# Optimization experiments

Hardware: AMD Instinct MI355X
Metric: run time of the kernel (lower is better)

## Reference

```python
import jax, jax.numpy as jnp
import numpy as np

D_MODEL = 1024
NHEAD = 16
HEAD_DIM = D_MODEL // NHEAD
D_FF = 4 * D_MODEL
B, L = 2, 2048
EPS = 1e-5


def layer_norm(x, g, b):
    mu = jnp.mean(x, axis=-1, keepdims=True)
    var = jnp.mean(jnp.square(x - mu), axis=-1, keepdims=True)
    return (x - mu) * jax.lax.rsqrt(var + EPS) * g + b


def setup_inputs() -> dict:
    key = jax.random.key(0)
    ks = jax.random.split(key, 12)
    s = 1.0 / np.sqrt(D_MODEL)
    inp = {
        "x": jax.random.normal(ks[0], (B, L, D_MODEL), jnp.float32),
        "mask": jnp.tril(jnp.ones((L, L), jnp.int32)),  # causal mask; 0 => masked
        "Wq": jax.random.normal(ks[1], (D_MODEL, D_MODEL), jnp.float32) * s,
        "bq": jnp.zeros((D_MODEL,), jnp.float32),
        "Wk": jax.random.normal(ks[2], (D_MODEL, D_MODEL), jnp.float32) * s,
        "bk": jnp.zeros((D_MODEL,), jnp.float32),
        "Wv": jax.random.normal(ks[3], (D_MODEL, D_MODEL), jnp.float32) * s,
        "bv": jnp.zeros((D_MODEL,), jnp.float32),
        "Wo": jax.random.normal(ks[4], (D_MODEL, D_MODEL), jnp.float32) * s,
        "bo": jnp.zeros((D_MODEL,), jnp.float32),
        "g1": jnp.ones((D_MODEL,), jnp.float32),
        "b1": jnp.zeros((D_MODEL,), jnp.float32),
        "g2": jnp.ones((D_MODEL,), jnp.float32),
        "b2": jnp.zeros((D_MODEL,), jnp.float32),
        "W1": jax.random.normal(ks[5], (D_MODEL, D_FF), jnp.float32) * s,
        "bf1": jnp.zeros((D_FF,), jnp.float32),
        "W2": jax.random.normal(ks[6], (D_FF, D_MODEL), jnp.float32) * (1.0 / np.sqrt(D_FF)),
        "bf2": jnp.zeros((D_MODEL,), jnp.float32),
    }
    return inp


def reference(x, mask, Wq, bq, Wk, bk, Wv, bv, Wo, bo, g1, b1, g2, b2, W1, bf1, W2, bf2):
    # Pre-norm attention (dropout = identity in eval mode)
    nx = layer_norm(x, g1, b1)
    Bb, Ll, Dd = nx.shape
    def heads(t):
        return t.reshape(Bb, Ll, NHEAD, HEAD_DIM).transpose(0, 2, 1, 3)  # [B,H,L,hd]
    q = heads(nx @ Wq + bq)
    k = heads(nx @ Wk + bk)
    v = heads(nx @ Wv + bv)
    scale = 1.0 / np.sqrt(HEAD_DIM)
    attn = jnp.einsum("bhqd,bhkd->bhqk", q, k) * scale  # [B,H,L,L]
    attn = jnp.where(mask[:Ll, :Ll] == 0, jnp.float32(-1e9), attn)
    attn = jax.nn.softmax(attn, axis=-1)
    attn_out = jnp.einsum("bhqk,bhkd->bhqd", attn, v)
    attn_out = attn_out.transpose(0, 2, 1, 3).reshape(Bb, Ll, Dd)
    x = x + (attn_out @ Wo + bo)
    # Pre-norm FFN with exact GELU (torch nn.GELU default)
    nx2 = layer_norm(x, g2, b2)
    h = jax.nn.gelu(nx2 @ W1 + bf1, approximate=False)
    x = x + (h @ W2 + bf2)
    return x
```

## Files before the change

### kernel.cpp

```cpp
#include <hip/hip_runtime.h>
#include <hip/hip_bf16.h>

__device__ __forceinline__ float bfbits2f(unsigned short u) {
  return __uint_as_float(((unsigned int)u) << 16);
}
__device__ __forceinline__ unsigned short f2bfbits(float f) {
  unsigned int x = __float_as_uint(f);
  unsigned int r = (x + 0x7FFFu + ((x >> 16) & 1u)) >> 16;
  return (unsigned short)r;
}

typedef short bf16x8 __attribute__((ext_vector_type(8)));
typedef float f32x4 __attribute__((ext_vector_type(4)));

__device__ __forceinline__ void gload_lds16(const unsigned short* g, unsigned short* l) {
  __builtin_amdgcn_global_load_lds((const __attribute__((address_space(1))) unsigned int*)g,
                                   (__attribute__((address_space(3))) unsigned int*)l, 16, 0, 0);
}

__global__ __launch_bounds__(256) void transpose_cast_k(const float* __restrict__ in,
                                                        unsigned short* __restrict__ out,
                                                        int K, int N) {
  __shared__ float tile[32][33];
  int n0 = blockIdx.x * 32, k0 = blockIdx.y * 32;
  int tx = threadIdx.x, ty = threadIdx.y;
#pragma unroll
  for (int j = 0; j < 32; j += 8)
    tile[ty + j][tx] = in[(size_t)(k0 + ty + j) * N + n0 + tx];
  __syncthreads();
#pragma unroll
  for (int j = 0; j < 32; j += 8)
    out[(size_t)(n0 + ty + j) * K + k0 + tx] = f2bfbits(tile[tx][ty + j]);
}

__global__ __launch_bounds__(256) void transpose_cast4_k(const float* __restrict__ w0,
                                                         const float* __restrict__ w1,
                                                         const float* __restrict__ w2,
                                                         const float* __restrict__ w3,
                                                         unsigned short* __restrict__ o012,
                                                         unsigned short* __restrict__ o3) {
  __shared__ float tile[32][33];
  int z = blockIdx.z;
  const float* in = (z == 0) ? w0 : (z == 1) ? w1 : (z == 2) ? w2 : w3;
  unsigned short* out = (z < 3) ? (o012 + (size_t)z * 1024 * 1024) : o3;
  int n0 = blockIdx.x * 32, k0 = blockIdx.y * 32;
  int tx = threadIdx.x, ty = threadIdx.y;
#pragma unroll
  for (int j = 0; j < 32; j += 8)
    tile[ty + j][tx] = in[(size_t)(k0 + ty + j) * 1024 + n0 + tx];
  __syncthreads();
#pragma unroll
  for (int j = 0; j < 32; j += 8)
    out[(size_t)(n0 + ty + j) * 1024 + k0 + tx] = f2bfbits(tile[tx][ty + j]);
}

__global__ void concat_bias_k(const float* __restrict__ bq, const float* __restrict__ bk,
                              const float* __restrict__ bv, float* __restrict__ out) {
  int i = blockIdx.x * 256 + threadIdx.x;
  if (i < 1024) {
    out[i] = bq[i];
    out[1024 + i] = bk[i];
    out[2048 + i] = bv[i];
  }
}

__global__ __launch_bounds__(256) void ln_k(const float* __restrict__ x,
                                            const float* __restrict__ g,
                                            const float* __restrict__ bb,
                                            unsigned short* __restrict__ out) {
  __shared__ float red[8];
  int row = blockIdx.x, tid = threadIdx.x;
  int lane = tid & 63, wv = tid >> 6;
  float4 v = reinterpret_cast<const float4*>(x + (size_t)row * 1024)[tid];
  float s = v.x + v.y + v.z + v.w;
#pragma unroll
  for (int off = 32; off >= 1; off >>= 1) s += __shfl_xor(s, off, 64);
  if (lane == 0) red[wv] = s;
  __syncthreads();
  float mu = (red[0] + red[1] + red[2] + red[3]) * (1.0f / 1024.0f);
  float a0 = v.x - mu, a1 = v.y - mu, a2 = v.z - mu, a3 = v.w - mu;
  float sq = a0 * a0 + a1 * a1 + a2 * a2 + a3 * a3;
#pragma unroll
  for (int off = 32; off >= 1; off >>= 1) sq += __shfl_xor(sq, off, 64);
  if (lane == 0) red[4 + wv] = sq;
  __syncthreads();
  float var = (red[4] + red[5] + red[6] + red[7]) * (1.0f / 1024.0f);
  float rstd = rsqrtf(var + 1e-5f);
  float4 gv = reinterpret_cast<const float4*>(g)[tid];
  float4 bv = reinterpret_cast<const float4*>(bb)[tid];
  ushort4 u;
  u.x = f2bfbits(a0 * rstd * gv.x + bv.x);
  u.y = f2bfbits(a1 * rstd * gv.y + bv.y);
  u.z = f2bfbits(a2 * rstd * gv.z + bv.z);
  u.w = f2bfbits(a3 * rstd * gv.w + bv.w);
  *reinterpret_cast<ushort4*>(out + (size_t)row * 1024 + tid * 4) = u;
}

template <int MODE>
__global__ __launch_bounds__(256) void gemm_bt_k(const unsigned short* __restrict__ A,
                                                 const unsigned short* __restrict__ BT,
                                                 const float* __restrict__ bias,
                                                 const float* __restrict__ resid,
                                                 void* __restrict__ Cout,
                                                 int M, int N, int K) {
  __shared__ unsigned short As[128 * 64];
  __shared__ unsigned short Bs[128 * 64];
  int tid = threadIdx.x;
  int wid = tid >> 6, lane = tid & 63;
  int m0 = blockIdx.x * 128, n0 = blockIdx.y * 128;
  int wr = wid >> 1, wc = wid & 1;
  int cl = lane & 15, g = lane >> 4;

  f32x4 acc[4][4];
#pragma unroll
  for (int i = 0; i < 4; i++)
#pragma unroll
    for (int j = 0; j < 4; j++) acc[i][j] = {0.f, 0.f, 0.f, 0.f};

  for (int k0 = 0; k0 < K; k0 += 64) {
#pragma unroll
    for (int i = 0; i < 4; ++i) {
      int c = i * 256 + tid;
      int r = c >> 3;
      int cc = (c & 7) * 8;
      gload_lds16(&A[(size_t)(m0 + r) * K + k0 + cc], &As[(i * 256 + wid * 64) * 8]);
      gload_lds16(&BT[(size_t)(n0 + r) * K + k0 + cc], &Bs[(i * 256 + wid * 64) * 8]);
    }
    __syncthreads();
#pragma unroll
    for (int kk = 0; kk < 64; kk += 32) {
      bf16x8 af[4], bfr[4];
#pragma unroll
      for (int mt = 0; mt < 4; mt++)
        af[mt] = *reinterpret_cast<const bf16x8*>(&As[(wr * 64 + mt * 16 + cl) * 64 + kk + g * 8]);
#pragma unroll
      for (int nt = 0; nt < 4; nt++)
        bfr[nt] = *reinterpret_cast<const bf16x8*>(&Bs[(wc * 64 + nt * 16 + cl) * 64 + kk + g * 8]);
#pragma unroll
      for (int mt = 0; mt < 4; mt++)
#pragma unroll
        for (int nt = 0; nt < 4; nt++)
          acc[mt][nt] = __builtin_amdgcn_mfma_f32_16x16x32_bf16(af[mt], bfr[nt], acc[mt][nt], 0, 0, 0);
    }
    __syncthreads();
  }

#pragma unroll
  for (int mt = 0; mt < 4; mt++) {
#pragma unroll
    for (int nt = 0; nt < 4; nt++) {
#pragma unroll
      for (int r = 0; r < 4; r++) {
        int gr = m0 + wr * 64 + mt * 16 + g * 4 + r;
        int gc = n0 + wc * 64 + nt * 16 + cl;
        float v = acc[mt][nt][r] + bias[gc];
        if constexpr (MODE == 1) {
          v += resid[(size_t)gr * N + gc];
          ((float*)Cout)[(size_t)gr * N + gc] = v;
        } else if constexpr (MODE == 2) {
          v = 0.5f * v * (1.0f + erff(v * 0.70710678118654752f));
          ((unsigned short*)Cout)[(size_t)gr * N + gc] = f2bfbits(v);
        } else {
          ((unsigned short*)Cout)[(size_t)gr * N + gc] = f2bfbits(v);
        }
      }
    }
  }
}

__global__ __launch_bounds__(512) void attn_k(const unsigned short* __restrict__ qkv,
                                              unsigned short* __restrict__ out) {
  __shared__ unsigned short Ks[2][64 * 64];
  __shared__ unsigned short Vt[64 * 64];
  __shared__ unsigned short Ps[8][16 * 64];

  const int L = 2048, RS = 3072;
  const float SCALE = 0.125f * 1.44269504f;
  int tid = threadIdx.x;
  int wid = tid >> 6, lane = tid & 63;
  int qt = (int)gridDim.x - 1 - (int)blockIdx.x;
  int h = blockIdx.y, b = blockIdx.z;
  int q0 = qt * 128;
  int qw = q0 + wid * 16;
  int g = lane >> 4;
  int cl = lane & 15;

  const unsigned short* kbase = qkv + (size_t)(b * L) * RS + 1024 + h * 64;
  const unsigned short* vbase = kbase + 1024;

  const unsigned short* qbase = qkv + (size_t)(b * L + qw + cl) * RS + h * 64 + g * 8;
  bf16x8 qf0 = *reinterpret_cast<const bf16x8*>(qbase);
  bf16x8 qf1 = *reinterpret_cast<const bf16x8*>(qbase + 32);

  int kr = tid >> 3, kch = tid & 7;
  size_t ksrc_off = (size_t)kr * RS + ((kch ^ (kr & 7)) * 8);
  int vk = tid & 63, vd0 = (tid >> 6) * 8;
  int vaddr[8];
#pragma unroll
  for (int j = 0; j < 8; ++j) {
    int d = vd0 + j;
    vaddr[j] = d * 64 + 8 * ((vk >> 3) ^ (d & 7)) + (vk & 7);
  }

  float m_r[4], l_r[4];
  f32x4 o_acc[4];
#pragma unroll
  for (int r = 0; r < 4; ++r) { m_r[r] = -1e30f; l_r[r] = 0.f; }
#pragma unroll
  for (int d = 0; d < 4; ++d) o_acc[d] = {0.f, 0.f, 0.f, 0.f};

  int nt = 2 * qt + 2;

  gload_lds16(kbase + ksrc_off, &Ks[0][wid * 512]);
  bf16x8 vreg = *reinterpret_cast<const bf16x8*>(vbase + (size_t)vk * RS + vd0);

  int buf = 0;
  for (int tt = 0; tt < nt; ++tt) {
    int kb = tt * 64;
    asm volatile("s_waitcnt vmcnt(0)" ::: "memory");
    __builtin_amdgcn_s_barrier();
    __builtin_amdgcn_sched_barrier(0);

#pragma unroll
    for (int j = 0; j < 8; ++j) Vt[vaddr[j]] = (unsigned short)vreg[j];

    if (tt + 1 < nt) {
      int kb1 = (size_t)(tt + 1) * 64;
      gload_lds16(kbase + (size_t)kb1 * RS + ksrc_off, &Ks[buf ^ 1][wid * 512]);
      vreg = *reinterpret_cast<const bf16x8*>(vbase + (size_t)(kb1 + vk) * RS + vd0);
    }

    f32x4 sacc[4];
#pragma unroll
    for (int kblk = 0; kblk < 4; ++kblk) sacc[kblk] = {0.f, 0.f, 0.f, 0.f};
#pragma unroll
    for (int kblk = 0; kblk < 4; ++kblk) {
      int kcol = kblk * 16 + cl;
      bf16x8 kf0 = *reinterpret_cast<const bf16x8*>(&Ks[buf][kcol * 64 + 8 * (g ^ (kcol & 7))]);
      bf16x8 kf1 = *reinterpret_cast<const bf16x8*>(&Ks[buf][kcol * 64 + 8 * ((g + 4) ^ (kcol & 7))]);
      sacc[kblk] = __builtin_amdgcn_mfma_f32_16x16x32_bf16(qf0, kf0, sacc[kblk], 0, 0, 0);
      sacc[kblk] = __builtin_amdgcn_mfma_f32_16x16x32_bf16(qf1, kf1, sacc[kblk], 0, 0, 0);
    }

    float rowmax[4];
    if (kb + 63 <= qw) {
#pragma unroll
      for (int r = 0; r < 4; ++r) {
        float mx = -1e30f;
#pragma unroll
        for (int kblk = 0; kblk < 4; ++kblk) {
          float s = sacc[kblk][r] * SCALE;
          sacc[kblk][r] = s;
          mx = fmaxf(mx, s);
        }
        rowmax[r] = mx;
      }
    } else {
#pragma unroll
      for (int r = 0; r < 4; ++r) {
        float mx = -1e30f;
        int qg = qw + g * 4 + r;
#pragma unroll
        for (int kblk = 0; kblk < 4; ++kblk) {
          float s = sacc[kblk][r] * SCALE;
          if (kb + kblk * 16 + cl > qg) s = -1e30f;
          sacc[kblk][r] = s;
          mx = fmaxf(mx, s);
        }
        rowmax[r] = mx;
      }
    }
#pragma unroll
    for (int off = 1; off <= 8; off <<= 1)
#pragma unroll
      for (int r = 0; r < 4; ++r) rowmax[r] = fmaxf(rowmax[r], __shfl_xor(rowmax[r], off, 64));
#pragma unroll
    for (int r = 0; r < 4; ++r) {
      float mnew = fmaxf(m_r[r], rowmax[r]);
      float corr = exp2f(m_r[r] - mnew);
      m_r[r] = mnew;
      int q_l = g * 4 + r;
      float rs = 0.f;
#pragma unroll
      for (int kblk = 0; kblk < 4; ++kblk) {
        float p = exp2f(sacc[kblk][r] - mnew);
        rs += p;
        int k_l = kblk * 16 + cl;
        Ps[wid][q_l * 64 + 8 * ((k_l >> 3) ^ (q_l & 7)) + (k_l & 7)] = f2bfbits(p);
      }
#pragma unroll
      for (int off = 1; off <= 8; off <<= 1) rs += __shfl_xor(rs, off, 64);
      l_r[r] = l_r[r] * corr + rs;
#pragma unroll
      for (int dblk = 0; dblk < 4; ++dblk) o_acc[dblk][r] *= corr;
    }

    asm volatile("s_waitcnt lgkmcnt(0)" ::: "memory");
    __builtin_amdgcn_s_barrier();
    __builtin_amdgcn_sched_barrier(0);

    bf16x8 pa0 = *reinterpret_cast<const bf16x8*>(&Ps[wid][cl * 64 + 8 * (g ^ (cl & 7))]);
    bf16x8 pa1 = *reinterpret_cast<const bf16x8*>(&Ps[wid][cl * 64 + 8 * ((g + 4) ^ (cl & 7))]);
#pragma unroll
    for (int dblk = 0; dblk < 4; ++dblk) {
      int d = dblk * 16 + cl;
      bf16x8 vb0 = *reinterpret_cast<const bf16x8*>(&Vt[d * 64 + 8 * (g ^ (d & 7))]);
      bf16x8 vb1 = *reinterpret_cast<const bf16x8*>(&Vt[d * 64 + 8 * ((g + 4) ^ (d & 7))]);
      o_acc[dblk] = __builtin_amdgcn_mfma_f32_16x16x32_bf16(pa0, vb0, o_acc[dblk], 0, 0, 0);
      o_acc[dblk] = __builtin_amdgcn_mfma_f32_16x16x32_bf16(pa1, vb1, o_acc[dblk], 0, 0, 0);
    }
    buf ^= 1;
  }

#pragma unroll
  for (int r = 0; r < 4; ++r) {
    float linv = 1.0f / l_r[r];
    int orow = qw + g * 4 + r;
    unsigned short* obase = out + (size_t)(b * L + orow) * 1024 + h * 64;
#pragma unroll
    for (int dblk = 0; dblk < 4; ++dblk)
      obase[dblk * 16 + cl] = f2bfbits(o_acc[dblk][r] * linv);
  }
}

extern "C" void kernel_launch(void* const* d_in, const int* in_sizes, int n_in,
                              void* d_out, int out_size, void* d_ws, size_t ws_size,
                              hipStream_t stream) {
  const float* x = (const float*)d_in[0];
  const float* Wq = (const float*)d_in[2];
  const float* bq = (const float*)d_in[3];
  const float* Wk = (const float*)d_in[4];
  const float* bk = (const float*)d_in[5];
  const float* Wv = (const float*)d_in[6];
  const float* bv = (const float*)d_in[7];
  const float* Wo = (const float*)d_in[8];
  const float* bo = (const float*)d_in[9];
  const float* g1 = (const float*)d_in[10];
  const float* b1 = (const float*)d_in[11];
  const float* g2 = (const float*)d_in[12];
  const float* b2 = (const float*)d_in[13];
  const float* W1 = (const float*)d_in[14];
  const float* bf1 = (const float*)d_in[15];
  const float* W2 = (const float*)d_in[16];
  const float* bf2 = (const float*)d_in[17];
  float* out = (float*)d_out;

  const int M = 4096;
  char* ws = (char*)d_ws;
  size_t off = 0;
  auto alloc = [&](size_t bytes) -> void* {
    void* p = ws + off;
    off += (bytes + 255) & ~(size_t)255;
    return p;
  };
  unsigned short* WqkvT = (unsigned short*)alloc((size_t)3072 * 1024 * 2);
  unsigned short* WoT = (unsigned short*)alloc((size_t)1024 * 1024 * 2);
  unsigned short* W1T = (unsigned short*)alloc((size_t)4096 * 1024 * 2);
  unsigned short* W2T = (unsigned short*)alloc((size_t)1024 * 4096 * 2);
  float* bqkv = (float*)alloc(3072 * 4);
  unsigned short* actA = (unsigned short*)alloc((size_t)M * 1024 * 2);
  unsigned short* actB = (unsigned short*)alloc((size_t)M * 4096 * 2);

  dim3 tb(32, 8);
  transpose_cast4_k<<<dim3(32, 32, 4), tb, 0, stream>>>(Wq, Wk, Wv, Wo, WqkvT, WoT);
  transpose_cast_k<<<dim3(128, 32), tb, 0, stream>>>(W1, W1T, 1024, 4096);
  transpose_cast_k<<<dim3(32, 128), tb, 0, stream>>>(W2, W2T, 4096, 1024);
  concat_bias_k<<<dim3(4), dim3(256), 0, stream>>>(bq, bk, bv, bqkv);

  ln_k<<<dim3(M), dim3(256), 0, stream>>>(x, g1, b1, actA);
  gemm_bt_k<0><<<dim3(M / 128, 3072 / 128), dim3(256), 0, stream>>>(actA, WqkvT, bqkv, nullptr, actB, M, 3072, 1024);
  attn_k<<<dim3(16, 16, 2), dim3(512), 0, stream>>>(actB, actA);
  gemm_bt_k<1><<<dim3(M / 128, 1024 / 128), dim3(256), 0, stream>>>(actA, WoT, bo, x, out, M, 1024, 1024);
  ln_k<<<dim3(M), dim3(256), 0, stream>>>(out, g2, b2, actA);
  gemm_bt_k<2><<<dim3(M / 128, 4096 / 128), dim3(256), 0, stream>>>(actA, W1T, bf1, nullptr, actB, M, 4096, 1024);
  gemm_bt_k<1><<<dim3(M / 128, 1024 / 128), dim3(256), 0, stream>>>(actB, W2T, bf2, out, out, M, 1024, 4096);
}
```

Baseline: 531.5 us.

## Rewrite attention with 32x32 MFMA, register-resident P via permlane swap

New measurement: 469.1 us. 11.7% less time.

```diff
diff --git a/kernel.cpp b/kernel.cpp
--- a/kernel.cpp
+++ b/kernel.cpp
@@ -12,6 +12,21 @@
 
 typedef short bf16x8 __attribute__((ext_vector_type(8)));
 typedef float f32x4 __attribute__((ext_vector_type(4)));
+typedef float f32x16 __attribute__((ext_vector_type(16)));
+typedef int i32x4 __attribute__((ext_vector_type(4)));
+
+__device__ __forceinline__ int cvtpk(float lo, float hi_) {
+  int r;
+  asm("v_cvt_pk_bf16_f32 %0, %1, %2" : "=v"(r) : "v"(lo), "v"(hi_));
+  return r;
+}
+__device__ __forceinline__ void plswap(int& a, int& b) {
+  asm("v_permlane32_swap_b32 %0, %1" : "+v"(a), "+v"(b));
+}
+__device__ __forceinline__ bf16x8 mk8(int a, int b, int c, int d) {
+  i32x4 t = {a, b, c, d};
+  return __builtin_bit_cast(bf16x8, t);
+}
 
 __device__ __forceinline__ void gload_lds16(const unsigned short* g, unsigned short* l) {
   __builtin_amdgcn_global_load_lds((const __attribute__((address_space(1))) unsigned int*)g,
@@ -168,11 +183,10 @@
   }
 }
 
-__global__ __launch_bounds__(512) void attn_k(const unsigned short* __restrict__ qkv,
+__global__ __launch_bounds__(256) void attn_k(const unsigned short* __restrict__ qkv,
                                               unsigned short* __restrict__ out) {
   __shared__ unsigned short Ks[2][64 * 64];
   __shared__ unsigned short Vt[64 * 64];
-  __shared__ unsigned short Ps[8][16 * 64];
 
   const int L = 2048, RS = 3072;
   const float SCALE = 0.125f * 1.44269504f;
@@ -181,38 +195,53 @@
   int qt = (int)gridDim.x - 1 - (int)blockIdx.x;
   int h = blockIdx.y, b = blockIdx.z;
   int q0 = qt * 128;
-  int qw = q0 + wid * 16;
-  int g = lane >> 4;
-  int cl = lane & 15;
+  int qw = q0 + wid * 32;
+  int ql = lane & 31;
+  int hi = lane >> 5;
+  int qg = qw + ql;
 
   const unsigned short* kbase = qkv + (size_t)(b * L) * RS + 1024 + h * 64;
   const unsigned short* vbase = kbase + 1024;
 
-  const unsigned short* qbase = qkv + (size_t)(b * L + qw + cl) * RS + h * 64 + g * 8;
-  bf16x8 qf0 = *reinterpret_cast<const bf16x8*>(qbase);
-  bf16x8 qf1 = *reinterpret_cast<const bf16x8*>(qbase + 32);
-
-  int kr = tid >> 3, kch = tid & 7;
-  size_t ksrc_off = (size_t)kr * RS + ((kch ^ (kr & 7)) * 8);
-  int vk = tid & 63, vd0 = (tid >> 6) * 8;
-  int vaddr[8];
+  bf16x8 qf[4];
+  {
+    const unsigned short* qp = qkv + (size_t)(b * L + qg) * RS + h * 64 + hi * 8;
+#pragma unroll
+    for (int s = 0; s < 4; ++s) {
+      bf16x8 qr = *reinterpret_cast<const bf16x8*>(qp + s * 16);
+      int w0 = cvtpk(bfbits2f((unsigned short)qr[0]) * SCALE, bfbits2f((unsigned short)qr[1]) * SCALE);
+      int w1 = cvtpk(bfbits2f((unsigned short)qr[2]) * SCALE, bfbits2f((unsigned short)qr[3]) * SCALE);
+      int w2 = cvtpk(bfbits2f((unsigned short)qr[4]) * SCALE, bfbits2f((unsigned short)qr[5]) * SCALE);
+      int w3 = cvtpk(bfbits2f((unsigned short)qr[6]) * SCALE, bfbits2f((unsigned short)qr[7]) * SCALE);
+      qf[s] = mk8(w0, w1, w2, w3);
+    }
+  }
+
+  int kr0 = tid >> 3, kc0 = tid & 7;
+  size_t koff0 = (size_t)kr0 * RS + ((kc0 ^ (kr0 & 7)) * 8);
+  int vkp = (tid & 31) * 2, vd0 = (tid >> 5) * 8;
+  int vwaddr[8];
 #pragma unroll
   for (int j = 0; j < 8; ++j) {
     int d = vd0 + j;
-    vaddr[j] = d * 64 + 8 * ((vk >> 3) ^ (d & 7)) + (vk & 7);
-  }
-
-  float m_r[4], l_r[4];
-  f32x4 o_acc[4];
-#pragma unroll
-  for (int r = 0; r < 4; ++r) { m_r[r] = -1e30f; l_r[r] = 0.f; }
-#pragma unroll
-  for (int d = 0; d < 4; ++d) o_acc[d] = {0.f, 0.f, 0.f, 0.f};
+    vwaddr[j] = d * 64 + (((vkp >> 3) ^ (d & 7)) << 3) + (vkp & 7);
+  }
+
+  float m_r = -3.0e38f, l_r = 0.f;
+  f32x16 oA, oB;
+#pragma unroll
+  for (int r = 0; r < 16; ++r) { oA[r] = 0.f; oB[r] = 0.f; }
 
   int nt = 2 * qt + 2;
 
-  gload_lds16(kbase + ksrc_off, &Ks[0][wid * 512]);
-  bf16x8 vreg = *reinterpret_cast<const bf16x8*>(vbase + (size_t)vk * RS + vd0);
+  gload_lds16(kbase + koff0, &Ks[0][(wid * 64) * 8]);
+  gload_lds16(kbase + koff0 + (size_t)32 * RS, &Ks[0][(256 + wid * 64) * 8]);
+  bf16x8 vr0, vr1;
+  {
+    const unsigned short* vp = vbase + (size_t)vkp * RS + vd0;
+    vr0 = *reinterpret_cast<const bf16x8*>(vp);
+    vr1 = *reinterpret_cast<const bf16x8*>(vp + RS);
+  }
 
   int buf = 0;
   for (int tt = 0; tt < nt; ++tt) {
@@ -222,104 +251,121 @@
     __builtin_amdgcn_sched_barrier(0);
 
 #pragma unroll
-    for (int j = 0; j < 8; ++j) Vt[vaddr[j]] = (unsigned short)vreg[j];
+    for (int j = 0; j < 8; ++j) {
+      unsigned int pk = (unsigned int)(unsigned short)vr0[j] |
+                        ((unsigned int)(unsigned short)vr1[j] << 16);
+      *reinterpret_cast<unsigned int*>(&Vt[vwaddr[j]]) = pk;
+    }
 
     if (tt + 1 < nt) {
-      int kb1 = (size_t)(tt + 1) * 64;
-      gload_lds16(kbase + (size_t)kb1 * RS + ksrc_off, &Ks[buf ^ 1][wid * 512]);
-      vreg = *reinterpret_cast<const bf16x8*>(vbase + (size_t)(kb1 + vk) * RS + vd0);
-    }
-
-    f32x4 sacc[4];
-#pragma unroll
-    for (int kblk = 0; kblk < 4; ++kblk) sacc[kblk] = {0.f, 0.f, 0.f, 0.f};
-#pragma unroll
-    for (int kblk = 0; kblk < 4; ++kblk) {
-      int kcol = kblk * 16 + cl;
-      bf16x8 kf0 = *reinterpret_cast<const bf16x8*>(&Ks[buf][kcol * 64 + 8 * (g ^ (kcol & 7))]);
-      bf16x8 kf1 = *reinterpret_cast<const bf16x8*>(&Ks[buf][kcol * 64 + 8 * ((g + 4) ^ (kcol & 7))]);
-      sacc[kblk] = __builtin_amdgcn_mfma_f32_16x16x32_bf16(qf0, kf0, sacc[kblk], 0, 0, 0);
-      sacc[kblk] = __builtin_amdgcn_mfma_f32_16x16x32_bf16(qf1, kf1, sacc[kblk], 0, 0, 0);
-    }
-
-    float rowmax[4];
-    if (kb + 63 <= qw) {
-#pragma unroll
-      for (int r = 0; r < 4; ++r) {
-        float mx = -1e30f;
-#pragma unroll
-        for (int kblk = 0; kblk < 4; ++kblk) {
-          float s = sacc[kblk][r] * SCALE;
-          sacc[kblk][r] = s;
-          mx = fmaxf(mx, s);
-        }
-        rowmax[r] = mx;
+      size_t kb1r = (size_t)(tt + 1) * 64 * RS;
+      gload_lds16(kbase + kb1r + koff0, &Ks[buf ^ 1][(wid * 64) * 8]);
+      gload_lds16(kbase + kb1r + koff0 + (size_t)32 * RS, &Ks[buf ^ 1][(256 + wid * 64) * 8]);
+      const unsigned short* vp = vbase + kb1r + (size_t)vkp * RS + vd0;
+      vr0 = *reinterpret_cast<const bf16x8*>(vp);
+      vr1 = *reinterpret_cast<const bf16x8*>(vp + RS);
+    }
+
+    f32x16 s0, s1;
+#pragma unroll
+    for (int r = 0; r < 16; ++r) { s0[r] = 0.f; s1[r] = 0.f; }
+#pragma unroll
+    for (int s = 0; s < 4; ++s) {
+      int ch = ((s * 2 + hi) ^ (ql & 7)) * 8;
+      bf16x8 ka0 = *reinterpret_cast<const bf16x8*>(&Ks[buf][ql * 64 + ch]);
+      bf16x8 ka1 = *reinterpret_cast<const bf16x8*>(&Ks[buf][(32 + ql) * 64 + ch]);
+      s0 = __builtin_amdgcn_mfma_f32_32x32x16_bf16(ka0, qf[s], s0, 0, 0, 0);
+      s1 = __builtin_amdgcn_mfma_f32_32x32x16_bf16(ka1, qf[s], s1, 0, 0, 0);
+    }
+
+    if (kb + 63 > qw) {
+#pragma unroll
+      for (int r = 0; r < 16; ++r) {
+        int ko = kb + (r & 3) + 8 * (r >> 2) + 4 * hi;
+        if (ko > qg) s0[r] = -3.0e38f;
+        if (ko + 32 > qg) s1[r] = -3.0e38f;
       }
-    } else {
-#pragma unroll
-      for (int r = 0; r < 4; ++r) {
-        float mx = -1e30f;
-        int qg = qw + g * 4 + r;
-#pragma unroll
-        for (int kblk = 0; kblk < 4; ++kblk) {
-          float s = sacc[kblk][r] * SCALE;
-          if (kb + kblk * 16 + cl > qg) s = -1e30f;
-          sacc[kblk][r] = s;
-          mx = fmaxf(mx, s);
-        }
-        rowmax[r] = mx;
-      }
-    }
-#pragma unroll
-    for (int off = 1; off <= 8; off <<= 1)
-#pragma unroll
-      for (int r = 0; r < 4; ++r) rowmax[r] = fmaxf(rowmax[r], __shfl_xor(rowmax[r], off, 64));
-#pragma unroll
-    for (int r = 0; r < 4; ++r) {
-      float mnew = fmaxf(m_r[r], rowmax[r]);
-      float corr = exp2f(m_r[r] - mnew);
-      m_r[r] = mnew;
-      int q_l = g * 4 + r;
-      float rs = 0.f;
-#pragma unroll
-      for (int kblk = 0; kblk < 4; ++kblk) {
-        float p = exp2f(sacc[kblk][r] - mnew);
-        rs += p;
-        int k_l = kblk * 16 + cl;
-        Ps[wid][q_l * 64 + 8 * ((k_l >> 3) ^ (q_l & 7)) + (k_l & 7)] = f2bfbits(p);
-      }
-#pragma unroll
-      for (int off = 1; off <= 8; off <<= 1) rs += __shfl_xor(rs, off, 64);
-      l_r[r] = l_r[r] * corr + rs;
-#pragma unroll
-      for (int dblk = 0; dblk < 4; ++dblk) o_acc[dblk][r] *= corr;
-    }
+    }
+
+#define MX4(v, i) fmaxf(fmaxf(v[i], v[i + 1]), fmaxf(v[i + 2], v[i + 3]))
+    float ma = fmaxf(fmaxf(MX4(s0, 0), MX4(s0, 4)), fmaxf(MX4(s0, 8), MX4(s0, 12)));
+    float mb = fmaxf(fmaxf(MX4(s1, 0), MX4(s1, 4)), fmaxf(MX4(s1, 8), MX4(s1, 12)));
+    float mx = fmaxf(ma, mb);
+    mx = fmaxf(mx, __shfl_xor(mx, 32, 64));
+    float mnew = fmaxf(m_r, mx);
+    float corr = exp2f(m_r - mnew);
+    m_r = mnew;
+#pragma unroll
+    for (int r = 0; r < 16; ++r) {
+      s0[r] = exp2f(s0[r] - mnew);
+      s1[r] = exp2f(s1[r] - mnew);
+    }
+#define SM4(v, i) ((v[i] + v[i + 1]) + (v[i + 2] + v[i + 3]))
+    float rs = ((SM4(s0, 0) + SM4(s0, 4)) + (SM4(s0, 8) + SM4(s0, 12))) +
+               ((SM4(s1, 0) + SM4(s1, 4)) + (SM4(s1, 8) + SM4(s1, 12)));
+    rs += __shfl_xor(rs, 32, 64);
+    l_r = l_r * corr + rs;
+#pragma unroll
+    for (int r = 0; r < 16; ++r) { oA[r] *= corr; oB[r] *= corr; }
+
+    int c0 = cvtpk(s0[0], s0[1]), c1 = cvtpk(s0[2], s0[3]);
+    int c2 = cvtpk(s0[4], s0[5]), c3 = cvtpk(s0[6], s0[7]);
+    int c4 = cvtpk(s0[8], s0[9]), c5 = cvtpk(s0[10], s0[11]);
+    int c6 = cvtpk(s0[12], s0[13]), c7 = cvtpk(s0[14], s0[15]);
+    plswap(c0, c2); plswap(c1, c3); plswap(c4, c6); plswap(c5, c7);
+    bf16x8 p00 = mk8(c0, c1, c2, c3);
+    bf16x8 p01 = mk8(c4, c5, c6, c7);
+    int d0 = cvtpk(s1[0], s1[1]), d1 = cvtpk(s1[2], s1[3]);
+    int d2 = cvtpk(s1[4], s1[5]), d3 = cvtpk(s1[6], s1[7]);
+    int d4 = cvtpk(s1[8], s1[9]), d5 = cvtpk(s1[10], s1[11]);
+    int d6 = cvtpk(s1[12], s1[13]), d7 = cvtpk(s1[14], s1[15]);
+    plswap(d0, d2); plswap(d1, d3); plswap(d4, d6); plswap(d5, d7);
+    bf16x8 p10 = mk8(d0, d1, d2, d3);
+    bf16x8 p11 = mk8(d4, d5, d6, d7);
 
     asm volatile("s_waitcnt lgkmcnt(0)" ::: "memory");
     __builtin_amdgcn_s_barrier();
     __builtin_amdgcn_sched_barrier(0);
 
-    bf16x8 pa0 = *reinterpret_cast<const bf16x8*>(&Ps[wid][cl * 64 + 8 * (g ^ (cl & 7))]);
-    bf16x8 pa1 = *reinterpret_cast<const bf16x8*>(&Ps[wid][cl * 64 + 8 * ((g + 4) ^ (cl & 7))]);
-#pragma unroll
-    for (int dblk = 0; dblk < 4; ++dblk) {
-      int d = dblk * 16 + cl;
-      bf16x8 vb0 = *reinterpret_cast<const bf16x8*>(&Vt[d * 64 + 8 * (g ^ (d & 7))]);
-      bf16x8 vb1 = *reinterpret_cast<const bf16x8*>(&Vt[d * 64 + 8 * ((g + 4) ^ (d & 7))]);
-      o_acc[dblk] = __builtin_amdgcn_mfma_f32_16x16x32_bf16(pa0, vb0, o_acc[dblk], 0, 0, 0);
-      o_acc[dblk] = __builtin_amdgcn_mfma_f32_16x16x32_bf16(pa1, vb1, o_acc[dblk], 0, 0, 0);
+#pragma unroll
+    for (int kt = 0; kt < 2; ++kt) {
+#pragma unroll
+      for (int ss = 0; ss < 2; ++ss) {
+        bf16x8 pf = (kt == 0) ? (ss == 0 ? p00 : p01) : (ss == 0 ? p10 : p11);
+        int ch = (((kt * 4 + ss * 2 + hi)) ^ (ql & 7)) * 8;
+        bf16x8 va0 = *reinterpret_cast<const bf16x8*>(&Vt[ql * 64 + ch]);
+        bf16x8 va1 = *reinterpret_cast<const bf16x8*>(&Vt[(32 + ql) * 64 + ch]);
+        oA = __builtin_amdgcn_mfma_f32_32x32x16_bf16(va0, pf, oA, 0, 0, 0);
+        oB = __builtin_amdgcn_mfma_f32_32x32x16_bf16(va1, pf, oB, 0, 0, 0);
+      }
     }
     buf ^= 1;
   }
 
-#pragma unroll
-  for (int r = 0; r < 4; ++r) {
-    float linv = 1.0f / l_r[r];
-    int orow = qw + g * 4 + r;
-    unsigned short* obase = out + (size_t)(b * L + orow) * 1024 + h * 64;
-#pragma unroll
-    for (int dblk = 0; dblk < 4; ++dblk)
-      obase[dblk * 16 + cl] = f2bfbits(o_acc[dblk][r] * linv);
+  float linv = 1.0f / l_r;
+  __syncthreads();
+  unsigned short* Olds = &Ks[0][0];
+  int q_l = wid * 32 + ql;
+  auto dump = [&](const f32x16& o, int dt) {
+#pragma unroll
+    for (int g2 = 0; g2 < 4; ++g2) {
+      int w0 = cvtpk(o[g2 * 4 + 0] * linv, o[g2 * 4 + 1] * linv);
+      int w1 = cvtpk(o[g2 * 4 + 2] * linv, o[g2 * 4 + 3] * linv);
+      int dd = dt * 32 + 8 * g2 + 4 * hi;
+      int ea = q_l * 64 + (((dd >> 3) ^ (q_l & 7)) << 3) + (dd & 7);
+      int2 wv = {w0, w1};
+      *reinterpret_cast<int2*>(&Olds[ea]) = wv;
+    }
+  };
+  dump(oA, 0);
+  dump(oB, 1);
+  __syncthreads();
+#pragma unroll
+  for (int rep = 0; rep < 4; ++rep) {
+    int row = rep * 32 + (tid >> 3);
+    int j = tid & 7;
+    bf16x8 vv = *reinterpret_cast<const bf16x8*>(&Olds[row * 64 + ((j ^ (row & 7)) << 3)]);
+    *reinterpret_cast<bf16x8*>(out + (size_t)(b * L + q0 + row) * 1024 + h * 64 + j * 8) = vv;
   }
 }
 
@@ -369,7 +415,7 @@
 
   ln_k<<<dim3(M), dim3(256), 0, stream>>>(x, g1, b1, actA);
   gemm_bt_k<0><<<dim3(M / 128, 3072 / 128), dim3(256), 0, stream>>>(actA, WqkvT, bqkv, nullptr, actB, M, 3072, 1024);
-  attn_k<<<dim3(16, 16, 2), dim3(512), 0, stream>>>(actB, actA);
+  attn_k<<<dim3(16, 16, 2), dim3(256), 0, stream>>>(actB, actA);
   gemm_bt_k<1><<<dim3(M / 128, 1024 / 128), dim3(256), 0, stream>>>(actA, WoT, bo, x, out, M, 1024, 1024);
   ln_k<<<dim3(M), dim3(256), 0, stream>>>(out, g2, b2, actA);
   gemm_bt_k<2><<<dim3(M / 128, 4096 / 128), dim3(256), 0, stream>>>(actA, W1T, bf1, nullptr, actB, M, 4096, 1024);
```
